# Kernel tuning notes

Hardware: AMD Instinct MI355X
Metric: run time of the kernel (lower is better)

## Reference

```python
import math
import jax, jax.numpy as jnp
import numpy as np

CHANNELS = 512
OUT_CHANNELS = 512
N_HEADS = 8
K_CHANNELS = CHANNELS // N_HEADS
WINDOW = 4


def _get_relative_embeddings(emb, length):
    # emb: [1, 2*WINDOW+1, d] -> [1, 2*length-1, d]
    max_rel = 2 * WINDOW + 1
    pad_length = max(0, length - (WINDOW + 1))
    start = max(0, WINDOW + 1 - length)
    end = max_rel + 2 * length - 1
    if pad_length > 0:
        emb = jnp.pad(emb, ((0, 0), (pad_length, pad_length), (0, 0)))
    return emb[:, start:end]


def _rel_to_abs(x):
    # x: [b, h, l, 2l-1] -> [b, h, l, l] via skewing trick
    b, h, l, _ = x.shape
    x = jnp.pad(x, ((0, 0), (0, 0), (0, 0), (0, 1)))
    x_flat = x.reshape(b, h, l * 2 * l)
    x_flat = jnp.pad(x_flat, ((0, 0), (0, 0), (0, l - 1)))
    return x_flat.reshape(b, h, l + 1, 2 * l - 1)[..., :l, l - 1:]


def _abs_to_rel(x):
    # x: [b, h, l, l] -> [b, h, l, 2l-1]
    b, h, l, _ = x.shape
    x = jnp.pad(x, ((0, 0), (0, 0), (0, 0), (0, l - 1)))
    x_flat = x.reshape(b, h, -1)
    x_flat = jnp.pad(x_flat, ((0, 0), (0, 0), (l, 0)))
    return x_flat.reshape(b, h, l, 2 * l)[..., 1:]


def setup_inputs() -> dict:
    key = jax.random.key(0)
    ks = jax.random.split(key, 12)
    B, T = 4, 1024
    w_std = 1.0 / math.sqrt(CHANNELS)
    rel_std = K_CHANNELS ** (-0.5)
    return {
        'x': jax.random.normal(ks[0], (B, T, CHANNELS), jnp.float32),
        'c': jax.random.normal(ks[1], (B, T, CHANNELS), jnp.float32),
        'Wq': jax.random.normal(ks[2], (CHANNELS, CHANNELS), jnp.float32) * w_std,
        'bq': jnp.zeros((CHANNELS,), jnp.float32),
        'Wk': jax.random.normal(ks[3], (CHANNELS, CHANNELS), jnp.float32) * w_std,
        'bk': jnp.zeros((CHANNELS,), jnp.float32),
        'Wv': jax.random.normal(ks[4], (CHANNELS, CHANNELS), jnp.float32) * w_std,
        'bv': jnp.zeros((CHANNELS,), jnp.float32),
        'Wo': jax.random.normal(ks[5], (CHANNELS, OUT_CHANNELS), jnp.float32) * w_std,
        'bo': jnp.zeros((OUT_CHANNELS,), jnp.float32),
        'emb_rel_k': jax.random.normal(ks[6], (1, 2 * WINDOW + 1, K_CHANNELS), jnp.float32) * rel_std,
        'emb_rel_v': jax.random.normal(ks[7], (1, 2 * WINDOW + 1, K_CHANNELS), jnp.float32) * rel_std,
    }


def reference(x, c, Wq, bq, Wk, bk, Wv, bv, Wo, bo, emb_rel_k, emb_rel_v):
    b, t_t, _ = x.shape
    t_s = c.shape[1]
    # 1x1 convs == pointwise dense projections
    q = x @ Wq + bq
    k = c @ Wk + bk
    v = c @ Wv + bv
    q = q.reshape(b, t_t, N_HEADS, K_CHANNELS).transpose(0, 2, 1, 3)
    k = k.reshape(b, t_s, N_HEADS, K_CHANNELS).transpose(0, 2, 1, 3)
    v = v.reshape(b, t_s, N_HEADS, K_CHANNELS).transpose(0, 2, 1, 3)
    q_scaled = q / math.sqrt(K_CHANNELS)
    scores = jnp.einsum('bhtd,bhsd->bhts', q_scaled, k)
    # relative position bias via skewing trick (heads_share=True -> rel emb head dim 1)
    rel_k = _get_relative_embeddings(emb_rel_k, t_s)[0]  # [2*t_s-1, d]
    rel_logits = jnp.einsum('bhtd,md->bhtm', q_scaled, rel_k)
    scores = scores + _rel_to_abs(rel_logits)
    p_attn = jax.nn.softmax(scores, axis=-1)
    out = jnp.einsum('bhts,bhsd->bhtd', p_attn, v)
    rel_w = _abs_to_rel(p_attn)  # [b, h, t, 2t-1]
    rel_v = _get_relative_embeddings(emb_rel_v, t_s)[0]  # [2*t_s-1, d]
    out = out + jnp.einsum('bhtm,md->bhtd', rel_w, rel_v)
    out = out.transpose(0, 2, 1, 3).reshape(b, t_t, CHANNELS)
    return out @ Wo + bo
```

## Files before the change

### kernel.cpp

```cpp
#include <hip/hip_runtime.h>
#include <hip/hip_bf16.h>

#define B_ 4
#define T_ 1024
#define C_ 512
#define H_ 8

typedef __attribute__((ext_vector_type(8))) short short8;
typedef __attribute__((ext_vector_type(4))) float floatx4;

__device__ __forceinline__ unsigned short f2bs(float f) {
    __hip_bfloat16 h = __float2bfloat16(f);
    return *(unsigned short*)&h;
}
__device__ __forceinline__ float bs2f(unsigned short u) {
    __hip_bfloat16 h;
    *(unsigned short*)&h = u;
    return __bfloat162float(h);
}

__device__ __forceinline__ void gload_lds16(const void* g, void* l) {
    __builtin_amdgcn_global_load_lds(
        (const __attribute__((address_space(1))) unsigned int*)g,
        (__attribute__((address_space(3))) unsigned int*)l, 16, 0, 0);
}

__global__ __launch_bounds__(256) void prep(
    const float* __restrict__ Wq, const float* __restrict__ Wk,
    const float* __restrict__ Wv, const float* __restrict__ Wo,
    unsigned short* __restrict__ WT)
{
    __shared__ unsigned short tileT[32][33];
    const int r = blockIdx.x, tid = threadIdx.x;
    const int w = r >> 8, tile = r & 255;
    const int k0 = (tile >> 4) * 32, n0 = (tile & 15) * 32;
    const float* W = (w == 0) ? Wq : (w == 1) ? Wk : (w == 2) ? Wv : Wo;
    unsigned short* out = WT + (size_t)w * 512 * 512;
    const int kk = tid >> 3, ns = (tid & 7) * 4;
    const float4 v = *(const float4*)&W[(size_t)(k0 + kk) * 512 + n0 + ns];
    tileT[ns + 0][kk] = f2bs(v.x);
    tileT[ns + 1][kk] = f2bs(v.y);
    tileT[ns + 2][kk] = f2bs(v.z);
    tileT[ns + 3][kk] = f2bs(v.w);
    __syncthreads();
    const int nn = tid >> 3, ks = (tid & 7) * 4;
    ushort4 o;
    o.x = tileT[nn][ks + 0]; o.y = tileT[nn][ks + 1];
    o.z = tileT[nn][ks + 2]; o.w = tileT[nn][ks + 3];
    *(ushort4*)&out[(size_t)(n0 + nn) * 512 + k0 + ks] = o;
}

__global__ __launch_bounds__(256) void qkv_mfma(
    const float* __restrict__ x, const float* __restrict__ cc,
    const unsigned short* __restrict__ WT,
    const float* __restrict__ bq, const float* __restrict__ bk,
    const float* __restrict__ bv,
    unsigned short* __restrict__ Qc, unsigned short* __restrict__ Kc,
    unsigned short* __restrict__ Vtg)
{
    const int z = blockIdx.z;
    const float* A32 = (z == 0) ? x : cc;
    const unsigned short* Bt = WT + (size_t)z * 262144;
    const float* bias = (z == 0) ? bq : (z == 1) ? bk : bv;
    const float scale = (z == 0) ? 0.125f : 1.0f;

    __shared__ __align__(16) unsigned short sA[2 * 128 * 32];
    __shared__ __align__(16) unsigned short sB[2 * 128 * 32];

    const int tid = threadIdx.x;
    const int wave = tid >> 6, lane = tid & 63;
    const int m0 = blockIdx.y * 128, n0 = blockIdx.x * 128;
    const int mrow = lane & 15, quad = lane >> 4, kgrp = quad * 8;
    const int mhalf = (wave & 1) * 64, noff = (wave >> 1) * 64;
    const int lrow = lane >> 2, lseg = (lane & 3) * 16;

    const int fr0 = tid >> 3;
    const int fc4 = (tid & 7) * 4;

    floatx4 acc[4][4];
    #pragma unroll
    for (int i = 0; i < 4; i++)
        #pragma unroll
        for (int j = 0; j < 4; j++)
            acc[i][j] = (floatx4){0.f, 0.f, 0.f, 0.f};

    float4 a4[4];
    #pragma unroll
    for (int p = 0; p < 4; p++)
        a4[p] = *(const float4*)&A32[(size_t)(m0 + fr0 + p * 32) * 512 + fc4];
    #pragma unroll
    for (int j = 0; j < 2; j++) {
        const int rB = wave * 32 + j * 16 + lrow;
        gload_lds16((const char*)Bt + ((size_t)(n0 + rB) * 512) * 2 + lseg,
                    &sB[(size_t)(wave * 32 + j * 16) * 32]);
    }
    #pragma unroll
    for (int p = 0; p < 4; p++) {
        ushort4 o;
        o.x = f2bs(a4[p].x); o.y = f2bs(a4[p].y);
        o.z = f2bs(a4[p].z); o.w = f2bs(a4[p].w);
        *(ushort4*)&sA[(fr0 + p * 32) * 32 + fc4] = o;
    }

    for (int ck = 0; ck < 16; ck++) {
        const int buf = ck & 1;
        __syncthreads();
        if (ck < 15) {
            const int k0 = (ck + 1) * 32;
            #pragma unroll
            for (int j = 0; j < 2; j++) {
                const int rB = wave * 32 + j * 16 + lrow;
                gload_lds16((const char*)Bt + ((size_t)(n0 + rB) * 512 + k0) * 2 + lseg,
                            &sB[(size_t)((buf ^ 1) * 128 + wave * 32 + j * 16) * 32]);
            }
            #pragma unroll
            for (int p = 0; p < 4; p++)
                a4[p] = *(const float4*)&A32[(size_t)(m0 + fr0 + p * 32) * 512 + k0 + fc4];
        }
        const unsigned short* sAb = sA + (size_t)buf * 128 * 32;
        const unsigned short* sBb = sB + (size_t)buf * 128 * 32;
        short8 af[4], bfv[4];
        #pragma unroll
        for (int i = 0; i < 4; i++)
            af[i] = *(const short8*)&sAb[(size_t)(mhalf + i * 16 + mrow) * 32 + kgrp];
        #pragma unroll
        for (int i = 0; i < 4; i++)
            bfv[i] = *(const short8*)&sBb[(size_t)(noff + i * 16 + mrow) * 32 + kgrp];
        #pragma unroll
        for (int mt = 0; mt < 4; mt++)
            #pragma unroll
            for (int nt = 0; nt < 4; nt++)
                acc[mt][nt] = __builtin_amdgcn_mfma_f32_16x16x32_bf16(
                    af[mt], bfv[nt], acc[mt][nt], 0, 0, 0);
        if (ck < 15) {
            unsigned short* dst = sA + (size_t)(buf ^ 1) * 128 * 32;
            #pragma unroll
            for (int p = 0; p < 4; p++) {
                ushort4 o;
                o.x = f2bs(a4[p].x); o.y = f2bs(a4[p].y);
                o.z = f2bs(a4[p].z); o.w = f2bs(a4[p].w);
                *(ushort4*)&dst[(fr0 + p * 32) * 32 + fc4] = o;
            }
        }
    }

    const int rowq = quad * 4;
    if (z < 2) {
        unsigned short* Y = (z == 0) ? Qc : Kc;
        #pragma unroll
        for (int nt = 0; nt < 4; nt++) {
            const int n = n0 + noff + nt * 16 + mrow;
            const float bv_ = bias[n];
            const int h = n >> 6, d = n & 63;
            #pragma unroll
            for (int mt = 0; mt < 4; mt++)
                #pragma unroll
                for (int r = 0; r < 4; r++) {
                    const int m = m0 + mhalf + mt * 16 + rowq + r;
                    const int bb = m >> 10, t = m & 1023;
                    Y[(((size_t)bb * H_ + h) * 1024 + t) * 64 + d] =
                        f2bs((acc[mt][nt][r] + bv_) * scale);
                }
        }
    } else {
        #pragma unroll
        for (int nt = 0; nt < 4; nt++) {
            const int n = n0 + noff + nt * 16 + mrow;
            const float bv_ = bias[n];
            const int h = n >> 6, d = n & 63;
            #pragma unroll
            for (int mt = 0; mt < 4; mt++) {
                const int m = m0 + mhalf + mt * 16 + rowq;
                const int bb = m >> 10, t = m & 1023;
                ushort4 o4;
                o4.x = f2bs(acc[mt][nt][0] + bv_);
                o4.y = f2bs(acc[mt][nt][1] + bv_);
                o4.z = f2bs(acc[mt][nt][2] + bv_);
                o4.w = f2bs(acc[mt][nt][3] + bv_);
                *(ushort4*)&Vtg[(((size_t)bb * H_ + h) * 64 + d) * 1024 + t] = o4;
            }
        }
    }
}

__global__ __launch_bounds__(256) void out_mfma(
    const unsigned short* __restrict__ AOb, const unsigned short* __restrict__ WoT,
    const float* __restrict__ bias, float* __restrict__ out)
{
    __shared__ __align__(16) unsigned short sA[2 * 128 * 32];
    __shared__ __align__(16) unsigned short sB[2 * 64 * 32];

    const int tid = threadIdx.x;
    const int wave = tid >> 6, lane = tid & 63;
    const int m0 = blockIdx.y * 128, n0 = blockIdx.x * 64;
    const int mrow = lane & 15, quad = lane >> 4, kgrp = quad * 8;
    const int mhalf = (wave & 1) * 64, noff = (wave >> 1) * 32;
    const int lrow = lane >> 2, lseg = (lane & 3) * 16;

    floatx4 acc[4][2];
    #pragma unroll
    for (int i = 0; i < 4; i++)
        #pragma unroll
        for (int j = 0; j < 2; j++)
            acc[i][j] = (floatx4){0.f, 0.f, 0.f, 0.f};

    auto stage = [&](int k0, int bufi) {
        #pragma unroll
        for (int j = 0; j < 2; j++) {
            const int rA = wave * 32 + j * 16 + lrow;
            gload_lds16((const char*)AOb + ((size_t)(m0 + rA) * 512 + k0) * 2 + lseg,
                        &sA[(size_t)(bufi * 128 + wave * 32 + j * 16) * 32]);
        }
        const int rB = wave * 16 + lrow;
        gload_lds16((const char*)WoT + ((size_t)(n0 + rB) * 512 + k0) * 2 + lseg,
                    &sB[(size_t)(bufi * 64 + wave * 16) * 32]);
    };

    stage(0, 0);
    for (int ck = 0; ck < 16; ck++) {
        const int buf = ck & 1;
        __syncthreads();
        if (ck < 15) stage((ck + 1) * 32, buf ^ 1);
        const unsigned short* sAb = sA + (size_t)buf * 128 * 32;
        const unsigned short* sBb = sB + (size_t)buf * 64 * 32;
        short8 af[4], bfv[2];
        #pragma unroll
        for (int i = 0; i < 4; i++)
            af[i] = *(const short8*)&sAb[(size_t)(mhalf + i * 16 + mrow) * 32 + kgrp];
        #pragma unroll
        for (int i = 0; i < 2; i++)
            bfv[i] = *(const short8*)&sBb[(size_t)(noff + i * 16 + mrow) * 32 + kgrp];
        #pragma unroll
        for (int mt = 0; mt < 4; mt++)
            #pragma unroll
            for (int nt = 0; nt < 2; nt++)
                acc[mt][nt] = __builtin_amdgcn_mfma_f32_16x16x32_bf16(
                    af[mt], bfv[nt], acc[mt][nt], 0, 0, 0);
    }

    const int rowq = quad * 4;
    #pragma unroll
    for (int nt = 0; nt < 2; nt++) {
        const int n = n0 + noff + nt * 16 + mrow;
        const float bv_ = bias[n];
        #pragma unroll
        for (int mt = 0; mt < 4; mt++)
            #pragma unroll
            for (int r = 0; r < 4; r++) {
                const int m = m0 + mhalf + mt * 16 + rowq + r;
                out[(size_t)m * 512 + n] = acc[mt][nt][r] + bv_;
            }
    }
}

__device__ __forceinline__ void attn_stage(
    const unsigned short* __restrict__ Kc, const unsigned short* __restrict__ Vtg,
    size_t qkbase, size_t vtbase, int s0, int wave, int ldrow, int gseg,
    unsigned short* KLb, unsigned short* VtLb)
{
    #pragma unroll
    for (int j = 0; j < 2; j++) {
        const int br = wave * 16 + j * 8;
        gload_lds16((const char*)Kc + (qkbase + (size_t)(s0 + br + ldrow) * 64) * 2 + gseg * 16,
                    &KLb[br * 64]);
        gload_lds16((const char*)Vtg + (vtbase + (size_t)(br + ldrow) * 1024 + s0) * 2 + gseg * 16,
                    &VtLb[br * 64]);
    }
}

__global__ __launch_bounds__(256) void attn_mfma(
    const unsigned short* __restrict__ Qc, const unsigned short* __restrict__ Kc,
    const unsigned short* __restrict__ Vtg,
    const float* __restrict__ rk, const float* __restrict__ rv,
    unsigned short* __restrict__ AOb)
{
    __shared__ __align__(16) unsigned short KL[2][64 * 64];
    __shared__ __align__(16) unsigned short VtL[2][64 * 64];
    __shared__ __align__(16) unsigned short PL[4][16 * 72];
    __shared__ float qbL[64 * 9];
    __shared__ float bandL[64 * 9];
    __shared__ float rvL[9 * 64];
    __shared__ float lL[64];

    const int tb = blockIdx.x, bh = blockIdx.y;
    const int b = bh >> 3, h = bh & 7;
    const int tid = threadIdx.x;
    const int wave = tid >> 6, lane = tid & 63;
    const int t0 = tb * 64;
    const int t0w = t0 + wave * 16;
    const size_t qkbase = (size_t)bh * T_ * 64;
    const size_t vtbase = (size_t)bh * 64 * T_;

    const int mrow = lane & 15;
    const int quad = lane >> 4;
    const int kgrp = quad * 8;
    const int x7 = mrow & 7;
    const int ldrow = lane >> 3;
    const int gseg = (lane & 7) ^ ldrow;

    attn_stage(Kc, Vtg, qkbase, vtbase, 0, wave, ldrow, gseg, &KL[0][0], &VtL[0][0]);

    for (int idx = tid; idx < 576; idx += 256) {
        bandL[idx] = 0.f;
        rvL[idx] = rv[idx];
        const int row = idx / 9, w = idx - row * 9;
        const unsigned short* qp = &Qc[qkbase + (size_t)(t0 + row) * 64];
        float s0a = 0.f, s1a = 0.f, s2a = 0.f, s3a = 0.f;
        #pragma unroll
        for (int d8 = 0; d8 < 8; d8 += 4) {
            const short8 q0 = *(const short8*)&qp[d8 * 8];
            const short8 q1 = *(const short8*)&qp[(d8 + 1) * 8];
            const short8 q2 = *(const short8*)&qp[(d8 + 2) * 8];
            const short8 q3 = *(const short8*)&qp[(d8 + 3) * 8];
            #pragma unroll
            for (int i = 0; i < 8; i++) {
                s0a = fmaf(bs2f((unsigned short)q0[i]), rk[w * 64 + d8 * 8 + i], s0a);
                s1a = fmaf(bs2f((unsigned short)q1[i]), rk[w * 64 + (d8 + 1) * 8 + i], s1a);
                s2a = fmaf(bs2f((unsigned short)q2[i]), rk[w * 64 + (d8 + 2) * 8 + i], s2a);
                s3a = fmaf(bs2f((unsigned short)q3[i]), rk[w * 64 + (d8 + 3) * 8 + i], s3a);
            }
        }
        qbL[idx] = (s0a + s1a) + (s2a + s3a);
    }

    const short8 aQ0 = *(const short8*)&Qc[qkbase + (size_t)(t0w + mrow) * 64 + kgrp];
    const short8 aQ1 = *(const short8*)&Qc[qkbase + (size_t)(t0w + mrow) * 64 + 32 + kgrp];

    floatx4 Oc[4];
    float lsA[4] = {0.f, 0.f, 0.f, 0.f};
    #pragma unroll
    for (int dt = 0; dt < 4; dt++) Oc[dt] = (floatx4){0.f, 0.f, 0.f, 0.f};

    unsigned short* Pw = &PL[wave][0];
    float* qbw = &qbL[wave * 16 * 9];
    float* bandw = &bandL[wave * 16 * 9];

    for (int ck = 0; ck < 16; ck++) {
        const int s0 = ck * 64;
        const int buf = ck & 1;
        __syncthreads();
        if (ck < 15)
            attn_stage(Kc, Vtg, qkbase, vtbase, s0 + 64, wave, ldrow, gseg,
                       &KL[buf ^ 1][0], &VtL[buf ^ 1][0]);

        floatx4 Sc[4];
        #pragma unroll
        for (int st = 0; st < 4; st++) {
            const int row = st * 16 + mrow;
            const short8 aK0 = *(const short8*)&KL[buf][row * 64 + (quad ^ x7) * 8];
            const short8 aK1 = *(const short8*)&KL[buf][row * 64 + ((4 + quad) ^ x7) * 8];
            floatx4 s4 = {0.f, 0.f, 0.f, 0.f};
            s4 = __builtin_amdgcn_mfma_f32_16x16x32_bf16(aK0, aQ0, s4, 0, 0, 0);
            s4 = __builtin_amdgcn_mfma_f32_16x16x32_bf16(aK1, aQ1, s4, 0, 0, 0);
            Sc[st] = s4;
        }

        #pragma unroll
        for (int st = 0; st < 4; st++) {
            const int diff = s0 + st * 16 - t0w;
            float p0, p1, p2, p3;
            if (diff >= -19 && diff <= 19) {
                #pragma unroll
                for (int r = 0; r < 4; r++) {
                    const int rel = diff + quad * 4 + r - mrow;
                    float sc = Sc[st][r];
                    const bool inband = (rel >= -4) && (rel <= 4);
                    if (inband) sc += qbw[mrow * 9 + rel + 4];
                    const float p = __expf(sc);
                    if (inband) bandw[mrow * 9 + rel + 4] = p;
                    Sc[st][r] = p;
                }
            } else {
                #pragma unroll
                for (int r = 0; r < 4; r++) Sc[st][r] = __expf(Sc[st][r]);
            }
            p0 = Sc[st][0]; p1 = Sc[st][1]; p2 = Sc[st][2]; p3 = Sc[st][3];
            lsA[st] += (p0 + p1) + (p2 + p3);
            ushort4 o4;
            o4.x = f2bs(p0); o4.y = f2bs(p1); o4.z = f2bs(p2); o4.w = f2bs(p3);
            *(ushort4*)&Pw[mrow * 72 + st * 16 + quad * 4] = o4;
        }

        #pragma unroll
        for (int c = 0; c < 2; c++) {
            const short8 aP = *(const short8*)&Pw[mrow * 72 + c * 32 + kgrp];
            #pragma unroll
            for (int dt = 0; dt < 4; dt++) {
                const int segl = (c * 4 + quad) ^ x7;
                const short8 bV = *(const short8*)&VtL[buf][(dt * 16 + mrow) * 64 + segl * 8];
                Oc[dt] = __builtin_amdgcn_mfma_f32_16x16x32_bf16(aP, bV, Oc[dt], 0, 0, 0);
            }
        }
    }

    float lv = (lsA[0] + lsA[1]) + (lsA[2] + lsA[3]);
    lv += __shfl_xor(lv, 16);
    lv += __shfl_xor(lv, 32);
    if (quad == 0) lL[wave * 16 + mrow] = lv;

    #pragma unroll
    for (int r = 0; r < 4; r++) {
        const int tl = quad * 4 + r;
        const float inv = 1.f / lL[wave * 16 + tl];
        #pragma unroll
        for (int w = 0; w < 9; w++) {
            const float p = bandw[tl * 9 + w];
            #pragma unroll
            for (int dt = 0; dt < 4; dt++)
                Oc[dt][r] = fmaf(p, rvL[w * 64 + dt * 16 + mrow], Oc[dt][r]);
        }
        const int t = t0w + tl;
        #pragma unroll
        for (int dt = 0; dt < 4; dt++)
            AOb[((size_t)b * 1024 + t) * 512 + h * 64 + dt * 16 + mrow] =
                f2bs(Oc[dt][r] * inv);
    }
}

extern "C" void kernel_launch(void* const* d_in, const int* in_sizes, int n_in,
                              void* d_out, int out_size, void* d_ws, size_t ws_size,
                              hipStream_t stream)
{
    const float* x  = (const float*)d_in[0];
    const float* c  = (const float*)d_in[1];
    const float* Wq = (const float*)d_in[2];
    const float* bq = (const float*)d_in[3];
    const float* Wk = (const float*)d_in[4];
    const float* bk = (const float*)d_in[5];
    const float* Wv = (const float*)d_in[6];
    const float* bv = (const float*)d_in[7];
    const float* Wo = (const float*)d_in[8];
    const float* bo = (const float*)d_in[9];
    const float* rk = (const float*)d_in[10];
    const float* rv = (const float*)d_in[11];

    unsigned short* WT  = (unsigned short*)d_ws;
    unsigned short* Qc  = WT + (size_t)4 * 512 * 512;
    unsigned short* Kc  = Qc + (size_t)32 * 1024 * 64;
    unsigned short* Vtg = Kc + (size_t)32 * 1024 * 64;
    unsigned short* AOb = Vtg + (size_t)32 * 1024 * 64;

    prep<<<1024, 256, 0, stream>>>(Wq, Wk, Wv, Wo, WT);
    qkv_mfma<<<dim3(4, 32, 3), 256, 0, stream>>>(x, c, WT, bq, bk, bv, Qc, Kc, Vtg);
    attn_mfma<<<dim3(16, 32), 256, 0, stream>>>(Qc, Kc, Vtg, rk, rv, AOb);
    out_mfma<<<dim3(8, 32), 256, 0, stream>>>(AOb, WT + (size_t)3 * 262144, bo, (float*)d_out);
}
```

Measured before the change: 151.5 us.

## Fuse K and V projections sharing the c tile, reorder attention grid

New measurement: 153.7 us. About the same (+1.4%).

```diff
diff --git a/kernel.cpp b/kernel.cpp
--- a/kernel.cpp
+++ b/kernel.cpp
@@ -59,98 +59,98 @@
     unsigned short* __restrict__ Vtg)
 {
     const int z = blockIdx.z;
-    const float* A32 = (z == 0) ? x : cc;
-    const unsigned short* Bt = WT + (size_t)z * 262144;
-    const float* bias = (z == 0) ? bq : (z == 1) ? bk : bv;
-    const float scale = (z == 0) ? 0.125f : 1.0f;
+    if (z == 0 && blockIdx.x >= 4) return;
 
     __shared__ __align__(16) unsigned short sA[2 * 128 * 32];
     __shared__ __align__(16) unsigned short sB[2 * 128 * 32];
 
     const int tid = threadIdx.x;
     const int wave = tid >> 6, lane = tid & 63;
-    const int m0 = blockIdx.y * 128, n0 = blockIdx.x * 128;
     const int mrow = lane & 15, quad = lane >> 4, kgrp = quad * 8;
-    const int mhalf = (wave & 1) * 64, noff = (wave >> 1) * 64;
+    const int mhalf = (wave & 1) * 64;
     const int lrow = lane >> 2, lseg = (lane & 3) * 16;
-
     const int fr0 = tid >> 3;
     const int fc4 = (tid & 7) * 4;
-
-    floatx4 acc[4][4];
-    #pragma unroll
-    for (int i = 0; i < 4; i++)
-        #pragma unroll
-        for (int j = 0; j < 4; j++)
-            acc[i][j] = (floatx4){0.f, 0.f, 0.f, 0.f};
-
-    float4 a4[4];
-    #pragma unroll
-    for (int p = 0; p < 4; p++)
-        a4[p] = *(const float4*)&A32[(size_t)(m0 + fr0 + p * 32) * 512 + fc4];
-    #pragma unroll
-    for (int j = 0; j < 2; j++) {
-        const int rB = wave * 32 + j * 16 + lrow;
-        gload_lds16((const char*)Bt + ((size_t)(n0 + rB) * 512) * 2 + lseg,
-                    &sB[(size_t)(wave * 32 + j * 16) * 32]);
-    }
-    #pragma unroll
-    for (int p = 0; p < 4; p++) {
-        ushort4 o;
-        o.x = f2bs(a4[p].x); o.y = f2bs(a4[p].y);
-        o.z = f2bs(a4[p].z); o.w = f2bs(a4[p].w);
-        *(ushort4*)&sA[(fr0 + p * 32) * 32 + fc4] = o;
-    }
-
-    for (int ck = 0; ck < 16; ck++) {
-        const int buf = ck & 1;
-        __syncthreads();
-        if (ck < 15) {
-            const int k0 = (ck + 1) * 32;
-            #pragma unroll
-            for (int j = 0; j < 2; j++) {
-                const int rB = wave * 32 + j * 16 + lrow;
-                gload_lds16((const char*)Bt + ((size_t)(n0 + rB) * 512 + k0) * 2 + lseg,
-                            &sB[(size_t)((buf ^ 1) * 128 + wave * 32 + j * 16) * 32]);
-            }
-            #pragma unroll
-            for (int p = 0; p < 4; p++)
-                a4[p] = *(const float4*)&A32[(size_t)(m0 + fr0 + p * 32) * 512 + k0 + fc4];
-        }
-        const unsigned short* sAb = sA + (size_t)buf * 128 * 32;
-        const unsigned short* sBb = sB + (size_t)buf * 128 * 32;
-        short8 af[4], bfv[4];
+    const int m0 = blockIdx.y * 128;
+
+    if (z == 0) {
+        const float* A32 = x;
+        const unsigned short* Bt = WT;
+        const int n0 = blockIdx.x * 128;
+        const int noff = (wave >> 1) * 64;
+
+        floatx4 acc[4][4];
         #pragma unroll
         for (int i = 0; i < 4; i++)
-            af[i] = *(const short8*)&sAb[(size_t)(mhalf + i * 16 + mrow) * 32 + kgrp];
-        #pragma unroll
-        for (int i = 0; i < 4; i++)
-            bfv[i] = *(const short8*)&sBb[(size_t)(noff + i * 16 + mrow) * 32 + kgrp];
-        #pragma unroll
-        for (int mt = 0; mt < 4; mt++)
-            #pragma unroll
-            for (int nt = 0; nt < 4; nt++)
-                acc[mt][nt] = __builtin_amdgcn_mfma_f32_16x16x32_bf16(
-                    af[mt], bfv[nt], acc[mt][nt], 0, 0, 0);
-        if (ck < 15) {
-            unsigned short* dst = sA + (size_t)(buf ^ 1) * 128 * 32;
-            #pragma unroll
-            for (int p = 0; p < 4; p++) {
-                ushort4 o;
-                o.x = f2bs(a4[p].x); o.y = f2bs(a4[p].y);
-                o.z = f2bs(a4[p].z); o.w = f2bs(a4[p].w);
-                *(ushort4*)&dst[(fr0 + p * 32) * 32 + fc4] = o;
-            }
-        }
-    }
-
-    const int rowq = quad * 4;
-    if (z < 2) {
-        unsigned short* Y = (z == 0) ? Qc : Kc;
+            #pragma unroll
+            for (int j = 0; j < 4; j++)
+                acc[i][j] = (floatx4){0.f, 0.f, 0.f, 0.f};
+
+        float4 a4[4];
+        #pragma unroll
+        for (int p = 0; p < 4; p++)
+            a4[p] = *(const float4*)&A32[(size_t)(m0 + fr0 + p * 32) * 512 + fc4];
+        #pragma unroll
+        for (int j = 0; j < 2; j++) {
+            const int rB = wave * 32 + j * 16 + lrow;
+            gload_lds16((const char*)Bt + ((size_t)(n0 + rB) * 512) * 2 + lseg,
+                        &sB[(size_t)(wave * 32 + j * 16) * 32]);
+        }
+        #pragma unroll
+        for (int p = 0; p < 4; p++) {
+            ushort4 o;
+            o.x = f2bs(a4[p].x); o.y = f2bs(a4[p].y);
+            o.z = f2bs(a4[p].z); o.w = f2bs(a4[p].w);
+            *(ushort4*)&sA[(fr0 + p * 32) * 32 + fc4] = o;
+        }
+
+        for (int ck = 0; ck < 16; ck++) {
+            const int buf = ck & 1;
+            __syncthreads();
+            if (ck < 15) {
+                const int k0 = (ck + 1) * 32;
+                #pragma unroll
+                for (int j = 0; j < 2; j++) {
+                    const int rB = wave * 32 + j * 16 + lrow;
+                    gload_lds16((const char*)Bt + ((size_t)(n0 + rB) * 512 + k0) * 2 + lseg,
+                                &sB[(size_t)((buf ^ 1) * 128 + wave * 32 + j * 16) * 32]);
+                }
+                #pragma unroll
+                for (int p = 0; p < 4; p++)
+                    a4[p] = *(const float4*)&A32[(size_t)(m0 + fr0 + p * 32) * 512 + k0 + fc4];
+            }
+            const unsigned short* sAb = sA + (size_t)buf * 128 * 32;
+            const unsigned short* sBb = sB + (size_t)buf * 128 * 32;
+            short8 af[4], bfv[4];
+            #pragma unroll
+            for (int i = 0; i < 4; i++)
+                af[i] = *(const short8*)&sAb[(size_t)(mhalf + i * 16 + mrow) * 32 + kgrp];
+            #pragma unroll
+            for (int i = 0; i < 4; i++)
+                bfv[i] = *(const short8*)&sBb[(size_t)((wave >> 1) * 64 + i * 16 + mrow) * 32 + kgrp];
+            #pragma unroll
+            for (int mt = 0; mt < 4; mt++)
+                #pragma unroll
+                for (int nt = 0; nt < 4; nt++)
+                    acc[mt][nt] = __builtin_amdgcn_mfma_f32_16x16x32_bf16(
+                        af[mt], bfv[nt], acc[mt][nt], 0, 0, 0);
+            if (ck < 15) {
+                unsigned short* dst = sA + (size_t)(buf ^ 1) * 128 * 32;
+                #pragma unroll
+                for (int p = 0; p < 4; p++) {
+                    ushort4 o;
+                    o.x = f2bs(a4[p].x); o.y = f2bs(a4[p].y);
+                    o.z = f2bs(a4[p].z); o.w = f2bs(a4[p].w);
+                    *(ushort4*)&dst[(fr0 + p * 32) * 32 + fc4] = o;
+                }
+            }
+        }
+
+        const int rowq = quad * 4;
         #pragma unroll
         for (int nt = 0; nt < 4; nt++) {
             const int n = n0 + noff + nt * 16 + mrow;
-            const float bv_ = bias[n];
+            const float bv_ = bq[n];
             const int h = n >> 6, d = n & 63;
             #pragma unroll
             for (int mt = 0; mt < 4; mt++)
@@ -158,25 +158,117 @@
                 for (int r = 0; r < 4; r++) {
                     const int m = m0 + mhalf + mt * 16 + rowq + r;
                     const int bb = m >> 10, t = m & 1023;
-                    Y[(((size_t)bb * H_ + h) * 1024 + t) * 64 + d] =
-                        f2bs((acc[mt][nt][r] + bv_) * scale);
+                    Qc[(((size_t)bb * H_ + h) * 1024 + t) * 64 + d] =
+                        f2bs((acc[mt][nt][r] + bv_) * 0.125f);
                 }
         }
     } else {
-        #pragma unroll
-        for (int nt = 0; nt < 4; nt++) {
+        const float* A32 = cc;
+        const unsigned short* Btk = WT + (size_t)1 * 262144;
+        const unsigned short* Btv = WT + (size_t)2 * 262144;
+        const int n0 = blockIdx.x * 64;
+        const int noff = (wave >> 1) * 32;
+        unsigned short* sBk = sB;
+        unsigned short* sBv = sB + 2 * 64 * 32;
+
+        floatx4 accK[4][2], accV[4][2];
+        #pragma unroll
+        for (int i = 0; i < 4; i++)
+            #pragma unroll
+            for (int j = 0; j < 2; j++) {
+                accK[i][j] = (floatx4){0.f, 0.f, 0.f, 0.f};
+                accV[i][j] = (floatx4){0.f, 0.f, 0.f, 0.f};
+            }
+
+        float4 a4[4];
+        #pragma unroll
+        for (int p = 0; p < 4; p++)
+            a4[p] = *(const float4*)&A32[(size_t)(m0 + fr0 + p * 32) * 512 + fc4];
+        {
+            const int rB = wave * 16 + lrow;
+            gload_lds16((const char*)Btk + ((size_t)(n0 + rB) * 512) * 2 + lseg,
+                        &sBk[(size_t)(wave * 16) * 32]);
+            gload_lds16((const char*)Btv + ((size_t)(n0 + rB) * 512) * 2 + lseg,
+                        &sBv[(size_t)(wave * 16) * 32]);
+        }
+        #pragma unroll
+        for (int p = 0; p < 4; p++) {
+            ushort4 o;
+            o.x = f2bs(a4[p].x); o.y = f2bs(a4[p].y);
+            o.z = f2bs(a4[p].z); o.w = f2bs(a4[p].w);
+            *(ushort4*)&sA[(fr0 + p * 32) * 32 + fc4] = o;
+        }
+
+        for (int ck = 0; ck < 16; ck++) {
+            const int buf = ck & 1;
+            __syncthreads();
+            if (ck < 15) {
+                const int k0 = (ck + 1) * 32;
+                const int rB = wave * 16 + lrow;
+                gload_lds16((const char*)Btk + ((size_t)(n0 + rB) * 512 + k0) * 2 + lseg,
+                            &sBk[(size_t)((buf ^ 1) * 64 + wave * 16) * 32]);
+                gload_lds16((const char*)Btv + ((size_t)(n0 + rB) * 512 + k0) * 2 + lseg,
+                            &sBv[(size_t)((buf ^ 1) * 64 + wave * 16) * 32]);
+                #pragma unroll
+                for (int p = 0; p < 4; p++)
+                    a4[p] = *(const float4*)&A32[(size_t)(m0 + fr0 + p * 32) * 512 + k0 + fc4];
+            }
+            const unsigned short* sAb = sA + (size_t)buf * 128 * 32;
+            const unsigned short* sBkb = sBk + (size_t)buf * 64 * 32;
+            const unsigned short* sBvb = sBv + (size_t)buf * 64 * 32;
+            short8 af[4], bk_[2], bv2[2];
+            #pragma unroll
+            for (int i = 0; i < 4; i++)
+                af[i] = *(const short8*)&sAb[(size_t)(mhalf + i * 16 + mrow) * 32 + kgrp];
+            #pragma unroll
+            for (int i = 0; i < 2; i++) {
+                bk_[i] = *(const short8*)&sBkb[(size_t)(noff + i * 16 + mrow) * 32 + kgrp];
+                bv2[i] = *(const short8*)&sBvb[(size_t)(noff + i * 16 + mrow) * 32 + kgrp];
+            }
+            #pragma unroll
+            for (int mt = 0; mt < 4; mt++)
+                #pragma unroll
+                for (int nt = 0; nt < 2; nt++) {
+                    accK[mt][nt] = __builtin_amdgcn_mfma_f32_16x16x32_bf16(
+                        af[mt], bk_[nt], accK[mt][nt], 0, 0, 0);
+                    accV[mt][nt] = __builtin_amdgcn_mfma_f32_16x16x32_bf16(
+                        af[mt], bv2[nt], accV[mt][nt], 0, 0, 0);
+                }
+            if (ck < 15) {
+                unsigned short* dst = sA + (size_t)(buf ^ 1) * 128 * 32;
+                #pragma unroll
+                for (int p = 0; p < 4; p++) {
+                    ushort4 o;
+                    o.x = f2bs(a4[p].x); o.y = f2bs(a4[p].y);
+                    o.z = f2bs(a4[p].z); o.w = f2bs(a4[p].w);
+                    *(ushort4*)&dst[(fr0 + p * 32) * 32 + fc4] = o;
+                }
+            }
+        }
+
+        const int rowq = quad * 4;
+        #pragma unroll
+        for (int nt = 0; nt < 2; nt++) {
             const int n = n0 + noff + nt * 16 + mrow;
-            const float bv_ = bias[n];
+            const float bk_ = bk[n];
+            const float bv_ = bv[n];
             const int h = n >> 6, d = n & 63;
             #pragma unroll
             for (int mt = 0; mt < 4; mt++) {
+                #pragma unroll
+                for (int r = 0; r < 4; r++) {
+                    const int m = m0 + mhalf + mt * 16 + rowq + r;
+                    const int bb = m >> 10, t = m & 1023;
+                    Kc[(((size_t)bb * H_ + h) * 1024 + t) * 64 + d] =
+                        f2bs(accK[mt][nt][r] + bk_);
+                }
                 const int m = m0 + mhalf + mt * 16 + rowq;
                 const int bb = m >> 10, t = m & 1023;
                 ushort4 o4;
-                o4.x = f2bs(acc[mt][nt][0] + bv_);
-                o4.y = f2bs(acc[mt][nt][1] + bv_);
-                o4.z = f2bs(acc[mt][nt][2] + bv_);
-                o4.w = f2bs(acc[mt][nt][3] + bv_);
+                o4.x = f2bs(accV[mt][nt][0] + bv_);
+                o4.y = f2bs(accV[mt][nt][1] + bv_);
+                o4.z = f2bs(accV[mt][nt][2] + bv_);
+                o4.w = f2bs(accV[mt][nt][3] + bv_);
                 *(ushort4*)&Vtg[(((size_t)bb * H_ + h) * 64 + d) * 1024 + t] = o4;
             }
         }
@@ -282,7 +374,7 @@
     __shared__ float rvL[9 * 64];
     __shared__ float lL[64];
 
-    const int tb = blockIdx.x, bh = blockIdx.y;
+    const int bh = blockIdx.x, tb = blockIdx.y;
     const int b = bh >> 3, h = bh & 7;
     const int tid = threadIdx.x;
     const int wave = tid >> 6, lane = tid & 63;
@@ -441,7 +533,7 @@
     unsigned short* AOb = Vtg + (size_t)32 * 1024 * 64;
 
     prep<<<1024, 256, 0, stream>>>(Wq, Wk, Wv, Wo, WT);
-    qkv_mfma<<<dim3(4, 32, 3), 256, 0, stream>>>(x, c, WT, bq, bk, bv, Qc, Kc, Vtg);
-    attn_mfma<<<dim3(16, 32), 256, 0, stream>>>(Qc, Kc, Vtg, rk, rv, AOb);
+    qkv_mfma<<<dim3(8, 32, 2), 256, 0, stream>>>(x, c, WT, bq, bk, bv, Qc, Kc, Vtg);
+    attn_mfma<<<dim3(32, 16), 256, 0, stream>>>(Qc, Kc, Vtg, rk, rv, AOb);
     out_mfma<<<dim3(8, 32), 256, 0, stream>>>(AOb, WT + (size_t)3 * 262144, bo, (float*)d_out);
 }
```
